# Performance work log

Measured on AMD Instinct MI355X. Metric: run time of the kernel, lower is better.

## Reference

```python
import jax, jax.numpy as jnp
import numpy as np

WS = 7      # window_size
SS = 3      # shift_size
NH = 12     # num_heads
HD = 32     # head_dim (dim // num_heads)


def _ln(x, g, b, eps=1e-5):
    mu = jnp.mean(x, axis=-1, keepdims=True)
    var = jnp.mean((x - mu) ** 2, axis=-1, keepdims=True)
    return (x - mu) * jax.lax.rsqrt(var + eps) * g + b


def setup_inputs() -> dict:
    key = jax.random.key(0)
    ks = jax.random.split(key, 8)
    b, h, w, c = 32, 56, 56, 384
    hid = 4 * c
    s = 0.02
    return {
        "x": jax.random.normal(ks[0], (b, h * w, c), jnp.float32),
        "h": h,
        "w": w,
        "g1": jnp.ones((c,), jnp.float32),
        "b1": jnp.zeros((c,), jnp.float32),
        "wqkv": jax.random.normal(ks[1], (c, 3 * c), jnp.float32) * s,
        "bqkv": jnp.zeros((3 * c,), jnp.float32),
        "wproj": jax.random.normal(ks[2], (c, c), jnp.float32) * s,
        "bproj": jnp.zeros((c,), jnp.float32),
        "g2": jnp.ones((c,), jnp.float32),
        "b2": jnp.zeros((c,), jnp.float32),
        "wfc1": jax.random.normal(ks[3], (c, hid), jnp.float32) * s,
        "bfc1": jnp.zeros((hid,), jnp.float32),
        "wfc2": jax.random.normal(ks[4], (hid, c), jnp.float32) * s,
        "bfc2": jnp.zeros((c,), jnp.float32),
    }


def _swin_block(x, h, w, g1, b1, wqkv, bqkv, wproj, bproj, g2, b2, wfc1, bfc1, wfc2, bfc2):
    b, l, c = x.shape
    shortcut = x
    xn = _ln(x, g1, b1).reshape(b, h, w, c)
    pad_h = (WS - h % WS) % WS
    pad_w = (WS - w % WS) % WS
    if pad_h > 0 or pad_w > 0:
        xn = jnp.pad(xn, ((0, 0), (0, pad_h), (0, pad_w), (0, 0)))
    hp, wp = xn.shape[1], xn.shape[2]
    if SS > 0:
        xn = jnp.roll(xn, (-SS, -SS), axis=(1, 2))
    # window partition -> [b*nw, ws*ws, c]
    win = xn.reshape(b, hp // WS, WS, wp // WS, WS, c)
    win = win.transpose(0, 1, 3, 2, 4, 5).reshape(-1, WS * WS, c)
    # window attention
    bnw, n, _ = win.shape
    qkv = (win @ wqkv + bqkv).reshape(bnw, n, 3, NH, HD)
    q, k, v = qkv[:, :, 0], qkv[:, :, 1], qkv[:, :, 2]  # [bnw, n, nh, hd]
    scale = HD ** -0.5
    attn = jnp.einsum("bqhd,bkhd->bhqk", q, k) * scale
    attn = jax.nn.softmax(attn, axis=-1)
    out = jnp.einsum("bhqk,bkhd->bqhd", attn, v).reshape(bnw, n, c)
    out = out @ wproj + bproj
    # window reverse
    xo = out.reshape(b, hp // WS, wp // WS, WS, WS, c)
    xo = xo.transpose(0, 1, 3, 2, 4, 5).reshape(b, hp, wp, c)
    if SS > 0:
        xo = jnp.roll(xo, (SS, SS), axis=(1, 2))
    if pad_h > 0 or pad_w > 0:
        xo = xo[:, :h, :w, :]
    xo = xo.reshape(b, h * w, c)
    xo = shortcut + xo
    # MLP with residual
    y = _ln(xo, g2, b2)
    y = jax.nn.gelu(y @ wfc1 + bfc1, approximate=False) @ wfc2 + bfc2
    return xo + y


def reference(x, h, w, g1, b1, wqkv, bqkv, wproj, bproj, g2, b2, wfc1, bfc1, wfc2, bfc2):
    return _swin_block(x, h, w, g1, b1, wqkv, bqkv, wproj, bproj,
                       g2, b2, wfc1, bfc1, wfc2, bfc2)
```

## Files before the change

### kernel.cpp

```cpp
#include <hip/hip_runtime.h>
#include <math.h>


typedef float f32x4 __attribute__((ext_vector_type(4)));
typedef float f32x2 __attribute__((ext_vector_type(2)));
typedef __bf16 bf16x8 __attribute__((ext_vector_type(8)));
typedef short s16x8 __attribute__((ext_vector_type(8)));
typedef unsigned short u16x2 __attribute__((ext_vector_type(2)));

#define DEV static __device__ __forceinline__

DEV unsigned short f2bf(float f) {
  unsigned int u = __builtin_bit_cast(unsigned int, f);
  u += 0x7fffu + ((u >> 16) & 1u);
  return (unsigned short)(u >> 16);
}
DEV float bf2f(unsigned short h) {
  unsigned int u = ((unsigned int)h) << 16;
  return __builtin_bit_cast(float, u);
}
DEV void load_lds16(const void* g, void* l) {
  __builtin_amdgcn_global_load_lds(
      (const __attribute__((address_space(1))) unsigned int*)g,
      (__attribute__((address_space(3))) unsigned int*)l, 16, 0, 0);
}

DEV int win_src_row(int row) {
  int win = row / 49, t = row - win * 49;
  int bimg = win >> 6, wrem = win & 63;
  int wy = wrem >> 3, wx = wrem & 7;
  int ti = t / 7, tj = t - ti * 7;
  int hh = wy * 7 + ti, ww = wx * 7 + tj;
  int sh = hh + 3; if (sh >= 56) sh -= 56;
  int sw = ww + 3; if (sw >= 56) sw -= 56;
  return bimg * 3136 + sh * 56 + sw;
}

__global__ void wt_kernel(const float* __restrict__ w, unsigned short* __restrict__ wt,
                          int Kd, int Nd) {
  int idx = blockIdx.x * 256 + threadIdx.x;
  if (idx >= Kd * Nd) return;
  int n = idx / Kd, k = idx - n * Kd;
  wt[idx] = f2bf(w[(size_t)k * Nd + n]);
}

template <int GATHER>
__global__ __launch_bounds__(256) void ln_kernel(const float* __restrict__ x,
                                                 const float* __restrict__ g,
                                                 const float* __restrict__ bb,
                                                 unsigned short* __restrict__ out) {
  int row = blockIdx.x * 4 + (threadIdx.x >> 6);
  int lane = threadIdx.x & 63;
  int src = GATHER ? win_src_row(row) : row;
  const float* xr = x + (size_t)src * 384;
  f32x2 p0 = *(const f32x2*)(xr + lane * 2);
  f32x2 p1 = *(const f32x2*)(xr + 128 + lane * 2);
  f32x2 p2 = *(const f32x2*)(xr + 256 + lane * 2);
  float s = p0.x + p0.y + p1.x + p1.y + p2.x + p2.y;
  float s2 = p0.x * p0.x + p0.y * p0.y + p1.x * p1.x + p1.y * p1.y +
             p2.x * p2.x + p2.y * p2.y;
#pragma unroll
  for (int off = 32; off; off >>= 1) {
    s += __shfl_xor(s, off);
    s2 += __shfl_xor(s2, off);
  }
  float mu = s * (1.0f / 384.0f);
  float rs = rsqrtf(s2 * (1.0f / 384.0f) - mu * mu + 1e-5f);
  unsigned short* orow = out + (size_t)row * 384;
  int c = lane * 2;
  u16x2 o;
  o.x = f2bf((p0.x - mu) * rs * g[c] + bb[c]);
  o.y = f2bf((p0.y - mu) * rs * g[c + 1] + bb[c + 1]);
  *(u16x2*)(orow + c) = o;
  c += 128;
  o.x = f2bf((p1.x - mu) * rs * g[c] + bb[c]);
  o.y = f2bf((p1.y - mu) * rs * g[c + 1] + bb[c + 1]);
  *(u16x2*)(orow + c) = o;
  c += 128;
  o.x = f2bf((p2.x - mu) * rs * g[c] + bb[c]);
  o.y = f2bf((p2.y - mu) * rs * g[c + 1] + bb[c + 1]);
  *(u16x2*)(orow + c) = o;
}

template <int EPI>
__global__ __launch_bounds__(512, 4) void gemmP(const unsigned short* __restrict__ A,
                                                const unsigned short* __restrict__ BT,
                                                const float* __restrict__ bias, int Kd,
                                                int nTilesN, void* __restrict__ out0,
                                                const float* __restrict__ res) {
  constexpr int BM = 256, BN = 128, BK = 32;
  __shared__ __attribute__((aligned(16))) unsigned short As[3][BM * BK];
  __shared__ __attribute__((aligned(16))) unsigned short Bs[3][BN * BK];
  const int tid = threadIdx.x;
  const int wid = tid >> 6, lane = tid & 63;
  const int nwg = gridDim.x;
  const int xcd = blockIdx.x & 7, loc = blockIdx.x >> 3;
  const int q = nwg >> 3, rr = nwg & 7;
  const int swz = (xcd < rr ? xcd * (q + 1) : rr * (q + 1) + (xcd - rr) * q) + loc;
  const int bm = swz / nTilesN, bn = swz - bm * nTilesN;
  const int wr = wid >> 1, wc = wid & 1;
  f32x4 acc[4][4] = {};
  const int srow = tid >> 2;
  const int chunk = (tid & 3) ^ ((tid >> 3) & 3);
  const unsigned short* gA0 = A + (size_t)(bm * BM + srow) * Kd + chunk * 8;
  const unsigned short* gB0 = BT + (size_t)(bn * BN + srow) * Kd + chunk * 8;
  const size_t rowstep = (size_t)128 * Kd;

  const int frow = lane & 15, g = lane >> 4;
  const int rslot = (g ^ ((frow >> 1) & 3)) << 3;
  const int aBase = (wr * 64 + frow) * BK + rslot;
  const int bBase = (wc * 64 + frow) * BK + rslot;

  const int nk = Kd >> 5;
  {
    unsigned short* lA = &As[0][tid * 8];
    load_lds16(gA0, lA);
    load_lds16(gA0 + rowstep, lA + 4096);
    load_lds16(gB0, &Bs[0][tid * 8]);
    unsigned short* lA1 = &As[1][tid * 8];
    load_lds16(gA0 + 32, lA1);
    load_lds16(gA0 + 32 + rowstep, lA1 + 4096);
    load_lds16(gB0 + 32, &Bs[1][tid * 8]);
  }
  asm volatile("s_waitcnt vmcnt(3)");
  __builtin_amdgcn_sched_barrier(0);
  __builtin_amdgcn_s_barrier();
  int b = 0;
  for (int t = 0; t < nk; ++t) {
    const int bst = (b == 0) ? 2 : b - 1;
    const int k0n = (t + 2) << 5;
    const unsigned short* Ab = As[b];
    const unsigned short* Bb = Bs[b];
    __builtin_amdgcn_sched_barrier(0);
    bf16x8 af[4], bfr[2];
#pragma unroll
    for (int m = 0; m < 4; m++) af[m] = *(const bf16x8*)(Ab + aBase + m * 16 * BK);
#pragma unroll
    for (int n = 0; n < 2; n++) bfr[n] = *(const bf16x8*)(Bb + bBase + n * 16 * BK);
    if (t + 2 < nk) {
      unsigned short* lA = &As[bst][tid * 8];
      load_lds16(gA0 + k0n, lA);
      load_lds16(gA0 + k0n + rowstep, lA + 4096);
    }
    __builtin_amdgcn_sched_barrier(0);
    __builtin_amdgcn_s_barrier();
    asm volatile("s_waitcnt lgkmcnt(0)");
    __builtin_amdgcn_sched_barrier(0);
    __builtin_amdgcn_s_setprio(1);
#pragma unroll
    for (int m = 0; m < 4; m++)
#pragma unroll
      for (int n = 0; n < 2; n++)
        acc[m][n] = __builtin_amdgcn_mfma_f32_16x16x32_bf16(af[m], bfr[n],
                                                            acc[m][n], 0, 0, 0);
    __builtin_amdgcn_s_setprio(0);
    __builtin_amdgcn_sched_barrier(0);
    __builtin_amdgcn_s_barrier();
    bf16x8 bfr2[2];
#pragma unroll
    for (int n = 0; n < 2; n++)
      bfr2[n] = *(const bf16x8*)(Bb + bBase + (n + 2) * 16 * BK);
    if (t + 2 < nk) load_lds16(gB0 + k0n, &Bs[bst][tid * 8]);
    __builtin_amdgcn_sched_barrier(0);
    __builtin_amdgcn_s_barrier();
    asm volatile("s_waitcnt lgkmcnt(0)");
    __builtin_amdgcn_sched_barrier(0);
    __builtin_amdgcn_s_setprio(1);
#pragma unroll
    for (int m = 0; m < 4; m++)
#pragma unroll
      for (int n = 0; n < 2; n++)
        acc[m][n + 2] = __builtin_amdgcn_mfma_f32_16x16x32_bf16(af[m], bfr2[n],
                                                                acc[m][n + 2], 0, 0, 0);
    __builtin_amdgcn_s_setprio(0);
    __builtin_amdgcn_sched_barrier(0);
    if (t + 1 < nk) {
      if (t + 2 < nk) asm volatile("s_waitcnt vmcnt(3)");
      else asm volatile("s_waitcnt vmcnt(0)");
      __builtin_amdgcn_sched_barrier(0);
    }
    __builtin_amdgcn_s_barrier();
    b = (b == 2) ? 0 : b + 1;
  }
  const int rbase = bm * BM + wr * 64 + (g << 2);
  const int cbase = bn * BN + wc * 64 + frow;
#pragma unroll
  for (int m = 0; m < 4; m++) {
#pragma unroll
    for (int j = 0; j < 4; j++) {
      const int r = rbase + m * 16 + j;
      if constexpr (EPI == 0) {
        unsigned short* C = (unsigned short*)out0;
        size_t ro = (size_t)r * 1152;
#pragma unroll
        for (int n = 0; n < 4; n++) {
          int cc = cbase + n * 16;
          C[ro + cc] = f2bf(acc[m][n][j] + bias[cc]);
        }
      } else if constexpr (EPI == 1) {
        float* XO = (float*)out0;
        size_t srowo = (size_t)win_src_row(r) * 384;
#pragma unroll
        for (int n = 0; n < 4; n++) {
          int cc = cbase + n * 16;
          XO[srowo + cc] = acc[m][n][j] + bias[cc] + res[srowo + cc];
        }
      } else if constexpr (EPI == 2) {
        unsigned short* H1 = (unsigned short*)out0;
        size_t ro = (size_t)r * 1536;
#pragma unroll
        for (int n = 0; n < 4; n++) {
          int cc = cbase + n * 16;
          float u = acc[m][n][j] + bias[cc];
          H1[ro + cc] = f2bf(0.5f * u * (1.0f + erff(u * 0.70710678118654752f)));
        }
      } else {
        float* O = (float*)out0;
        size_t ro = (size_t)r * 384;
#pragma unroll
        for (int n = 0; n < 4; n++) {
          int cc = cbase + n * 16;
          O[ro + cc] = acc[m][n][j] + bias[cc] + res[ro + cc];
        }
      }
    }
  }
}

__global__ __launch_bounds__(256) void attn_mfma(const unsigned short* __restrict__ QKV,
                                                 unsigned short* __restrict__ AO) {
  __shared__ __attribute__((aligned(16))) unsigned short L[4][7168];
  const int wid = threadIdx.x >> 6, lane = threadIdx.x & 63;
  const int blk = blockIdx.x * 4 + wid;
  const int win = blk / 12, head = blk - win * 12;
  unsigned short* Qs = L[wid];
  unsigned short* Ks = Qs + 2048;
  unsigned short* VT = Qs + 4096;
  unsigned short* Ps = Qs + 6144;
  const unsigned short* Qp = QKV + (size_t)win * 49 * 1152 + head * 32;
  for (int i = lane; i < 196; i += 64) {
    int row = i >> 2, c8 = (i & 3) << 3;
    const unsigned short* base = Qp + (size_t)row * 1152 + c8;
    *(s16x8*)(Qs + row * 32 + c8) = *(const s16x8*)(base);
    *(s16x8*)(Ks + row * 32 + c8) = *(const s16x8*)(base + 384);
    s16x8 vv = *(const s16x8*)(base + 768);
#pragma unroll
    for (int u = 0; u < 8; u++) VT[(c8 + u) * 64 + row] = (unsigned short)vv[u];
  }
  if (lane < 60) {
    s16x8 z = {};
    *(s16x8*)(Qs + 1568 + lane * 8) = z;
    *(s16x8*)(Ks + 1568 + lane * 8) = z;
  }
  for (int i = lane; i < 480; i += 64) {
    int d = i / 15, k = 49 + (i - d * 15);
    VT[d * 64 + k] = 0;
  }
  __syncthreads();

  const int g = lane >> 4, qi = lane & 15;
  const float scale = 0.17677669529663689f;
  bf16x8 kf[4];
#pragma unroll
  for (int mt = 0; mt < 4; mt++)
    kf[mt] = *(const bf16x8*)(Ks + (mt * 16 + qi) * 32 + g * 8);

  for (int nt = 0; nt < 4; nt++) {
    bf16x8 qf = *(const bf16x8*)(Qs + (nt * 16 + qi) * 32 + g * 8);
    f32x4 st[4];
#pragma unroll
    for (int mt = 0; mt < 4; mt++) {
      f32x4 zz = {};
      st[mt] = __builtin_amdgcn_mfma_f32_16x16x32_bf16(kf[mt], qf, zz, 0, 0, 0);
    }
    float m = -1e30f;
#pragma unroll
    for (int mt = 0; mt < 3; mt++)
#pragma unroll
      for (int j = 0; j < 4; j++) m = fmaxf(m, st[mt][j]);
    if (g == 0) m = fmaxf(m, st[3][0]);
    m = fmaxf(m, __shfl_xor(m, 16));
    m = fmaxf(m, __shfl_xor(m, 32));
    m *= scale;
    float p[4][4];
    float sum = 0.f;
#pragma unroll
    for (int mt = 0; mt < 4; mt++)
#pragma unroll
      for (int j = 0; j < 4; j++) {
        int k = mt * 16 + g * 4 + j;
        float e = (k < 49) ? __expf(st[mt][j] * scale - m) : 0.f;
        p[mt][j] = e;
        sum += e;
      }
    sum += __shfl_xor(sum, 16);
    sum += __shfl_xor(sum, 32);
    float inv = 1.0f / sum;
#pragma unroll
    for (int mt = 0; mt < 4; mt++)
#pragma unroll
      for (int j = 0; j < 4; j += 2) {
        unsigned int pk = (unsigned int)f2bf(p[mt][j]) |
                          ((unsigned int)f2bf(p[mt][j + 1]) << 16);
        *(unsigned int*)(Ps + qi * 64 + mt * 16 + g * 4 + j) = pk;
      }
    __syncthreads();
    f32x4 acc0 = {}, acc1 = {};
#pragma unroll
    for (int kt = 0; kt < 2; kt++) {
      bf16x8 pa = *(const bf16x8*)(Ps + qi * 64 + kt * 32 + g * 8);
      bf16x8 vb0 = *(const bf16x8*)(VT + qi * 64 + kt * 32 + g * 8);
      bf16x8 vb1 = *(const bf16x8*)(VT + (16 + qi) * 64 + kt * 32 + g * 8);
      acc0 = __builtin_amdgcn_mfma_f32_16x16x32_bf16(pa, vb0, acc0, 0, 0, 0);
      acc1 = __builtin_amdgcn_mfma_f32_16x16x32_bf16(pa, vb1, acc1, 0, 0, 0);
    }
#pragma unroll
    for (int jr = 0; jr < 4; jr++) {
      int q2 = g * 4 + jr;
      int qg = nt * 16 + q2;
      float iv = __shfl(inv, q2);
      if (qg < 49) {
        unsigned short* op = AO + ((size_t)win * 49 + qg) * 384 + head * 32 + qi;
        op[0] = f2bf(acc0[jr] * iv);
        op[16] = f2bf(acc1[jr] * iv);
      }
    }
    __syncthreads();
  }
}

extern "C" void kernel_launch(void* const* d_in, const int* in_sizes, int n_in,
                              void* d_out, int out_size, void* d_ws, size_t ws_size,
                              hipStream_t stream) {
  (void)in_sizes; (void)n_in; (void)out_size; (void)ws_size;
  const float* x = (const float*)d_in[0];
  const float* g1 = (const float*)d_in[3];
  const float* b1 = (const float*)d_in[4];
  const float* wqkv = (const float*)d_in[5];
  const float* bqkv = (const float*)d_in[6];
  const float* wproj = (const float*)d_in[7];
  const float* bproj = (const float*)d_in[8];
  const float* g2 = (const float*)d_in[9];
  const float* b2 = (const float*)d_in[10];
  const float* wfc1 = (const float*)d_in[11];
  const float* bfc1 = (const float*)d_in[12];
  const float* wfc2 = (const float*)d_in[13];
  const float* bfc2 = (const float*)d_in[14];

  char* ws = (char*)d_ws;
  unsigned short* wqkvT = (unsigned short*)ws;
  unsigned short* wprojT = wqkvT + 442368;
  unsigned short* wfc1T = wprojT + 147456;
  unsigned short* wfc2T = wfc1T + 589824;
  unsigned short* XW = wfc2T + 589824;
  unsigned short* QKV = XW + 38535168;
  unsigned short* AOb = XW;
  unsigned short* XN2 = QKV;
  unsigned short* H1buf = QKV + 38535168;
  float* XO = (float*)d_out;
  float* out = (float*)d_out;

  wt_kernel<<<1728, 256, 0, stream>>>(wqkv, wqkvT, 384, 1152);
  wt_kernel<<<576, 256, 0, stream>>>(wproj, wprojT, 384, 384);
  wt_kernel<<<2304, 256, 0, stream>>>(wfc1, wfc1T, 384, 1536);
  wt_kernel<<<2304, 256, 0, stream>>>(wfc2, wfc2T, 1536, 384);

  ln_kernel<1><<<25088, 256, 0, stream>>>(x, g1, b1, XW);
  gemmP<0><<<392 * 9, 512, 0, stream>>>(XW, wqkvT, bqkv, 384, 9, QKV, nullptr);
  attn_mfma<<<6144, 256, 0, stream>>>(QKV, AOb);
  gemmP<1><<<392 * 3, 512, 0, stream>>>(AOb, wprojT, bproj, 384, 3, XO, x);
  ln_kernel<0><<<25088, 256, 0, stream>>>(XO, g2, b2, XN2);
  for (int ch = 0; ch < 2; ch++) {
    const unsigned short* a2 = XN2 + (size_t)ch * 50176 * 384;
    float* o2 = out + (size_t)ch * 50176 * 384;
    gemmP<2><<<196 * 12, 512, 0, stream>>>(a2, wfc1T, bfc1, 384, 12, H1buf, nullptr);
    gemmP<3><<<196 * 3, 512, 0, stream>>>(H1buf, wfc2T, bfc2, 1536, 3, o2, o2);
  }
}
```

Measured before the change: 909.6 us.

## Add 256x256 BK64 GEMM kernel and route QKV and MLP GEMMs through it

Introduces gemm8p, a 256x256-tile bf16 MFMA GEMM with a 64-wide K step, double-buffered LDS and an XOR-swizzled layout. It is used for the QKV, fc1 and fc2 GEMMs, and the existing 256x128 kernel covers the leftover N columns (the last 128 columns of QKV and of fc2). The larger tile raises arithmetic intensity and reuse per block, cutting global and LDS traffic. In exchange it uses more registers and LDS, so fewer blocks fit per CU, and each GEMM now needs two launches, with some tail imbalance.

```diff
diff --git a/kernel.cpp b/kernel.cpp
--- a/kernel.cpp
+++ b/kernel.cpp
@@ -80,6 +80,167 @@
   o.x = f2bf((p2.x - mu) * rs * g[c] + bb[c]);
   o.y = f2bf((p2.y - mu) * rs * g[c + 1] + bb[c + 1]);
   *(u16x2*)(orow + c) = o;
+}
+
+template <int EPI>
+__global__ __launch_bounds__(512, 2) void gemm8p(const unsigned short* __restrict__ A,
+                                                 const unsigned short* __restrict__ BT,
+                                                 const float* __restrict__ bias, int Kd,
+                                                 int nTilesN, void* __restrict__ out0,
+                                                 const float* __restrict__ res) {
+  __shared__ __attribute__((aligned(16))) unsigned short As[2][16384];
+  __shared__ __attribute__((aligned(16))) unsigned short Bs[2][16384];
+  const int tid = threadIdx.x;
+  const int wid = tid >> 6, lane = tid & 63;
+  const int nwg = gridDim.x;
+  const int xcd = blockIdx.x & 7, loc = blockIdx.x >> 3;
+  const int q = nwg >> 3, rr = nwg & 7;
+  const int swz = (xcd < rr ? xcd * (q + 1) : rr * (q + 1) + (xcd - rr) * q) + loc;
+  const int bm = swz / nTilesN, bn = swz - bm * nTilesN;
+  const int wr = wid >> 2, wc = wid & 3;
+  f32x4 acc[8][4] = {};
+  const int srow = tid >> 3;
+  const int sslot = (tid & 7) ^ (srow & 7);
+  const unsigned short* gA0 = A + (size_t)(bm * 256 + srow) * Kd + sslot * 8;
+  const unsigned short* gB0 = BT + (size_t)(bn * 256 + srow) * Kd + sslot * 8;
+  const size_t rowstep = (size_t)64 * Kd;
+
+  auto STAGE_A = [&](int bb, int t) {
+    const int k0 = t << 6;
+#pragma unroll
+    for (int s = 0; s < 4; s++)
+      load_lds16(gA0 + k0 + s * rowstep, &As[bb][s * 4096 + tid * 8]);
+  };
+  auto STAGE_B = [&](int bb, int t) {
+    const int k0 = t << 6;
+#pragma unroll
+    for (int s = 0; s < 4; s++)
+      load_lds16(gB0 + k0 + s * rowstep, &Bs[bb][s * 4096 + tid * 8]);
+  };
+
+  const int frow = lane & 15, g = lane >> 4, fx = frow & 7;
+  const int aRowBase = (wr * 128 + frow) * 64;
+  const int bRowBase = (wc * 64 + frow) * 64;
+  const int s0 = (g ^ fx) * 8;
+  const int s1 = ((4 | g) ^ fx) * 8;
+
+  const int nk = Kd >> 6;
+  STAGE_A(0, 0);
+  STAGE_B(0, 0);
+  asm volatile("s_waitcnt vmcnt(0)");
+  __builtin_amdgcn_sched_barrier(0);
+  __builtin_amdgcn_s_barrier();
+  for (int t = 0; t < nk; ++t) {
+    const int b = t & 1, nb = b ^ 1;
+    const unsigned short* Ab = As[b];
+    const unsigned short* Bb = Bs[b];
+    bf16x8 af[8], bf[2];
+    __builtin_amdgcn_sched_barrier(0);
+#pragma unroll
+    for (int m = 0; m < 8; m++) af[m] = *(const bf16x8*)(Ab + aRowBase + m * 1024 + s0);
+#pragma unroll
+    for (int n = 0; n < 2; n++) bf[n] = *(const bf16x8*)(Bb + bRowBase + n * 1024 + s0);
+    if (t + 1 < nk) STAGE_A(nb, t + 1);
+    __builtin_amdgcn_sched_barrier(0);
+    __builtin_amdgcn_s_barrier();
+    asm volatile("s_waitcnt lgkmcnt(0)");
+    __builtin_amdgcn_sched_barrier(0);
+    __builtin_amdgcn_s_setprio(1);
+#pragma unroll
+    for (int m = 0; m < 8; m++)
+#pragma unroll
+      for (int n = 0; n < 2; n++)
+        acc[m][n] = __builtin_amdgcn_mfma_f32_16x16x32_bf16(af[m], bf[n], acc[m][n], 0, 0, 0);
+    __builtin_amdgcn_s_setprio(0);
+    __builtin_amdgcn_sched_barrier(0);
+    __builtin_amdgcn_s_barrier();
+    bf16x8 bf2[2];
+#pragma unroll
+    for (int n = 0; n < 2; n++) bf2[n] = *(const bf16x8*)(Bb + bRowBase + (n + 2) * 1024 + s0);
+    if (t + 1 < nk) STAGE_B(nb, t + 1);
+    __builtin_amdgcn_sched_barrier(0);
+    __builtin_amdgcn_s_barrier();
+    asm volatile("s_waitcnt lgkmcnt(0)");
+    __builtin_amdgcn_sched_barrier(0);
+    __builtin_amdgcn_s_setprio(1);
+#pragma unroll
+    for (int m = 0; m < 8; m++)
+#pragma unroll
+      for (int n = 0; n < 2; n++)
+        acc[m][n + 2] = __builtin_amdgcn_mfma_f32_16x16x32_bf16(af[m], bf2[n], acc[m][n + 2], 0, 0, 0);
+    __builtin_amdgcn_s_setprio(0);
+    __builtin_amdgcn_sched_barrier(0);
+    __builtin_amdgcn_s_barrier();
+#pragma unroll
+    for (int m = 0; m < 8; m++) af[m] = *(const bf16x8*)(Ab + aRowBase + m * 1024 + s1);
+#pragma unroll
+    for (int n = 0; n < 2; n++) bf[n] = *(const bf16x8*)(Bb + bRowBase + n * 1024 + s1);
+    __builtin_amdgcn_sched_barrier(0);
+    __builtin_amdgcn_s_barrier();
+    asm volatile("s_waitcnt lgkmcnt(0)");
+    __builtin_amdgcn_sched_barrier(0);
+    __builtin_amdgcn_s_setprio(1);
+#pragma unroll
+    for (int m = 0; m < 8; m++)
+#pragma unroll
+      for (int n = 0; n < 2; n++)
+        acc[m][n] = __builtin_amdgcn_mfma_f32_16x16x32_bf16(af[m], bf[n], acc[m][n], 0, 0, 0);
+    __builtin_amdgcn_s_setprio(0);
+    __builtin_amdgcn_sched_barrier(0);
+    __builtin_amdgcn_s_barrier();
+#pragma unroll
+    for (int n = 0; n < 2; n++) bf2[n] = *(const bf16x8*)(Bb + bRowBase + (n + 2) * 1024 + s1);
+    __builtin_amdgcn_sched_barrier(0);
+    __builtin_amdgcn_s_barrier();
+    asm volatile("s_waitcnt lgkmcnt(0)");
+    __builtin_amdgcn_sched_barrier(0);
+    __builtin_amdgcn_s_setprio(1);
+#pragma unroll
+    for (int m = 0; m < 8; m++)
+#pragma unroll
+      for (int n = 0; n < 2; n++)
+        acc[m][n + 2] = __builtin_amdgcn_mfma_f32_16x16x32_bf16(af[m], bf2[n], acc[m][n + 2], 0, 0, 0);
+    __builtin_amdgcn_s_setprio(0);
+    __builtin_amdgcn_sched_barrier(0);
+    asm volatile("s_waitcnt vmcnt(0)");
+    __builtin_amdgcn_sched_barrier(0);
+    __builtin_amdgcn_s_barrier();
+  }
+  const int rbase = bm * 256 + wr * 128 + (g << 2);
+  const int cbase = bn * 256 + wc * 64 + frow;
+#pragma unroll
+  for (int m = 0; m < 8; m++) {
+#pragma unroll
+    for (int j = 0; j < 4; j++) {
+      const int r = rbase + m * 16 + j;
+      if constexpr (EPI == 0) {
+        unsigned short* C = (unsigned short*)out0;
+        size_t ro = (size_t)r * 1152;
+#pragma unroll
+        for (int n = 0; n < 4; n++) {
+          int cc = cbase + n * 16;
+          C[ro + cc] = f2bf(acc[m][n][j] + bias[cc]);
+        }
+      } else if constexpr (EPI == 2) {
+        unsigned short* H1 = (unsigned short*)out0;
+        size_t ro = (size_t)r * 1536;
+#pragma unroll
+        for (int n = 0; n < 4; n++) {
+          int cc = cbase + n * 16;
+          float u = acc[m][n][j] + bias[cc];
+          H1[ro + cc] = f2bf(0.5f * u * (1.0f + erff(u * 0.70710678118654752f)));
+        }
+      } else {
+        float* O = (float*)out0;
+        size_t ro = (size_t)r * 384;
+#pragma unroll
+        for (int n = 0; n < 4; n++) {
+          int cc = cbase + n * 16;
+          O[ro + cc] = acc[m][n][j] + bias[cc] + res[ro + cc];
+        }
+      }
+    }
+  }
 }
 
 template <int EPI>
@@ -106,6 +267,14 @@
   const unsigned short* gB0 = BT + (size_t)(bn * BN + srow) * Kd + chunk * 8;
   const size_t rowstep = (size_t)128 * Kd;
 
+  auto STAGE = [&](int b, int t) {
+    const int k0 = t << 5;
+    unsigned short* lA = &As[b][tid * 8];
+    load_lds16(gA0 + k0, lA);
+    load_lds16(gA0 + k0 + rowstep, lA + 4096);
+    load_lds16(gB0 + k0, &Bs[b][tid * 8]);
+  };
+
   const int frow = lane & 15, g = lane >> 4;
   const int rslot = (g ^ ((frow >> 1) & 3)) << 3;
   const int aBase = (wr * 64 + frow) * BK + rslot;
@@ -151,8 +320,7 @@
     for (int m = 0; m < 4; m++)
 #pragma unroll
       for (int n = 0; n < 2; n++)
-        acc[m][n] = __builtin_amdgcn_mfma_f32_16x16x32_bf16(af[m], bfr[n],
-                                                            acc[m][n], 0, 0, 0);
+        acc[m][n] = __builtin_amdgcn_mfma_f32_16x16x32_bf16(af[m], bfr[n], acc[m][n], 0, 0, 0);
     __builtin_amdgcn_s_setprio(0);
     __builtin_amdgcn_sched_barrier(0);
     __builtin_amdgcn_s_barrier();
@@ -170,8 +338,7 @@
     for (int m = 0; m < 4; m++)
 #pragma unroll
       for (int n = 0; n < 2; n++)
-        acc[m][n + 2] = __builtin_amdgcn_mfma_f32_16x16x32_bf16(af[m], bfr2[n],
-                                                                acc[m][n + 2], 0, 0, 0);
+        acc[m][n + 2] = __builtin_amdgcn_mfma_f32_16x16x32_bf16(af[m], bfr2[n], acc[m][n + 2], 0, 0, 0);
     __builtin_amdgcn_s_setprio(0);
     __builtin_amdgcn_sched_barrier(0);
     if (t + 1 < nk) {
@@ -204,15 +371,6 @@
         for (int n = 0; n < 4; n++) {
           int cc = cbase + n * 16;
           XO[srowo + cc] = acc[m][n][j] + bias[cc] + res[srowo + cc];
-        }
-      } else if constexpr (EPI == 2) {
-        unsigned short* H1 = (unsigned short*)out0;
-        size_t ro = (size_t)r * 1536;
-#pragma unroll
-        for (int n = 0; n < 4; n++) {
-          int cc = cbase + n * 16;
-          float u = acc[m][n][j] + bias[cc];
-          H1[ro + cc] = f2bf(0.5f * u * (1.0f + erff(u * 0.70710678118654752f)));
         }
       } else {
         float* O = (float*)out0;
@@ -366,14 +524,18 @@
   wt_kernel<<<2304, 256, 0, stream>>>(wfc2, wfc2T, 1536, 384);
 
   ln_kernel<1><<<25088, 256, 0, stream>>>(x, g1, b1, XW);
-  gemmP<0><<<392 * 9, 512, 0, stream>>>(XW, wqkvT, bqkv, 384, 9, QKV, nullptr);
+  gemm8p<0><<<392 * 4, 512, 0, stream>>>(XW, wqkvT, bqkv, 384, 4, QKV, nullptr);
+  gemmP<0><<<392, 512, 0, stream>>>(XW, wqkvT + 1024 * 384, bqkv + 1024, 384, 1,
+                                    QKV + 1024, nullptr);
   attn_mfma<<<6144, 256, 0, stream>>>(QKV, AOb);
   gemmP<1><<<392 * 3, 512, 0, stream>>>(AOb, wprojT, bproj, 384, 3, XO, x);
   ln_kernel<0><<<25088, 256, 0, stream>>>(XO, g2, b2, XN2);
   for (int ch = 0; ch < 2; ch++) {
     const unsigned short* a2 = XN2 + (size_t)ch * 50176 * 384;
     float* o2 = out + (size_t)ch * 50176 * 384;
-    gemmP<2><<<196 * 12, 512, 0, stream>>>(a2, wfc1T, bfc1, 384, 12, H1buf, nullptr);
-    gemmP<3><<<196 * 3, 512, 0, stream>>>(H1buf, wfc2T, bfc2, 1536, 3, o2, o2);
-  }
-}
+    gemm8p<2><<<196 * 6, 512, 0, stream>>>(a2, wfc1T, bfc1, 384, 6, H1buf, nullptr);
+    gemm8p<3><<<196, 512, 0, stream>>>(H1buf, wfc2T, bfc2, 1536, 1, o2, o2);
+    gemmP<3><<<196, 512, 0, stream>>>(H1buf, wfc2T + 256 * 1536, bfc2 + 256, 1536, 1,
+                                      o2 + 256, o2 + 256);
+  }
+}
```

After: 1.043 ms. 14.6% more time.
